# Performance work log

Hardware: AMD Instinct MI355X
Metric: run time of the kernel (lower is better)

Reference implementation:

```python
import jax, jax.numpy as jnp
import numpy as np

KQ_D = 64  # head dim from init_kwargs

def setup_inputs() -> dict:
    key = jax.random.key(0)
    k1, k2, k3, k4 = jax.random.split(key, 4)
    B, H, S, D = 2, 12, 2048, KQ_D
    q = jax.random.normal(k1, (B, H, S, D), dtype=jnp.float32)
    k = jax.random.normal(k2, (B, H, S, D), dtype=jnp.float32)
    v = jax.random.normal(k3, (B, H, S, D), dtype=jnp.float32)
    mask = jax.random.randint(k4, (B, 1, S, S), 0, 2, dtype=jnp.int32)
    return {"q": q, "k": k, "v": v, "mask": mask}

def reference(q, k, v, mask):
    # attn = (q @ k^T) / sqrt(kq_d)
    scale = 1.0 / (KQ_D ** 0.5)
    attn = jnp.einsum('bhqd,bhkd->bhqk', q, k) * scale
    # masked_fill(mask == 0, -1e9)
    attn = jnp.where(mask == 0, jnp.float32(-1e9), attn)
    # softmax over keys; dropout is identity in eval/reference mode
    attn = jax.nn.softmax(attn, axis=-1)
    out = jnp.einsum('bhqk,bhkd->bhqd', attn, v)
    return out
```

## Files before the change

kernel.cpp:

```cpp
#include <hip/hip_runtime.h>
#include <hip/hip_bf16.h>

#define S_LEN 2048
#define D_DIM 64
#define NH    12
#define NB    2
#define BH_N  (NB*NH)
#define TILES 32
#define TILE_BYTES 16384
#define KV_WS_BYTES ((size_t)BH_N * TILES * TILE_BYTES)
#define MASK_WORDS  ((size_t)NB * S_LEN * TILES)
#define WS_NEEDED   (KV_WS_BYTES + MASK_WORDS * 8)

typedef __attribute__((ext_vector_type(8))) short short8;
typedef __attribute__((ext_vector_type(4))) float f32x4;
typedef __attribute__((ext_vector_type(16))) float f32x16;

static __device__ inline unsigned bfbits(float f) {
    __hip_bfloat16 h = __float2bfloat16(f);
    return (unsigned)*reinterpret_cast<const unsigned short*>(&h);
}

static __device__ inline void gload_lds16(const void* g, unsigned ldsoff) {
    __builtin_amdgcn_global_load_lds(
        (__attribute__((address_space(1))) void*)(unsigned long long)(uintptr_t)g,
        (__attribute__((address_space(3))) void*)(unsigned long long)ldsoff,
        16, 0, 0);
}

__global__ __launch_bounds__(256) void prep(const float* __restrict__ k,
                                            const float* __restrict__ v,
                                            const int* __restrict__ mask,
                                            char* __restrict__ wsKV,
                                            unsigned long long* __restrict__ wm) {
    __shared__ __align__(16) float sv[64 * 68];
    const int tid = threadIdx.x;
    const int bid = blockIdx.x;
    if (bid < 768) {
        const int t = bid & 31, bh = bid >> 5;
        const int kv0 = t * 64;
        const float* kb = k + (size_t)bh * (S_LEN * D_DIM);
        const float* vb = v + (size_t)bh * (S_LEN * D_DIM);
        char* img = wsKV + ((size_t)bh * TILES + t) * TILE_BYTES;

#pragma unroll
        for (int g = 0; g < 4; ++g) {
            int i = g * 256 + tid;
            int row = i >> 4, cb = (i & 15) << 3;
            int cp = cb ^ ((row & 7) << 4);
            float4 f = *(const float4*)(kb + (size_t)(kv0 + row) * D_DIM + (cp >> 1));
            uint2 u;
            u.x = bfbits(f.x) | (bfbits(f.y) << 16);
            u.y = bfbits(f.z) | (bfbits(f.w) << 16);
            *(uint2*)(img + (size_t)i * 8) = u;
            float4 fv = *(const float4*)(vb + (size_t)(kv0 + row) * D_DIM + ((i & 15) << 2));
            *(float4*)&sv[row * 68 + ((i & 15) << 2)] = fv;
        }
        __syncthreads();
#pragma unroll
        for (int g = 0; g < 4; ++g) {
            int i = g * 256 + tid;
            int drow = i >> 4, cb = (i & 15) << 3;
            int cp = cb ^ ((drow & 7) << 4);
            int key0 = cp >> 1;
            uint2 u;
            u.x = bfbits(sv[(key0 + 0) * 68 + drow]) | (bfbits(sv[(key0 + 1) * 68 + drow]) << 16);
            u.y = bfbits(sv[(key0 + 2) * 68 + drow]) | (bfbits(sv[(key0 + 3) * 68 + drow]) << 16);
            *(uint2*)(img + 8192 + (size_t)i * 8) = u;
        }
    } else {
        const int lane = tid & 63;
        const int wgid = (bid - 768) * 4 + (tid >> 6);
#pragma unroll 1
        for (int g = 0; g < 16; ++g) {
            const int t0 = wgid * 64 + g * 4;
            const size_t base = (size_t)t0 * 64 + lane;
            int m0 = mask[base];
            int m1 = mask[base + 64];
            int m2 = mask[base + 128];
            int m3 = mask[base + 192];
            unsigned long long b0 = __ballot(m0 != 0);
            unsigned long long b1 = __ballot(m1 != 0);
            unsigned long long b2 = __ballot(m2 != 0);
            unsigned long long b3 = __ballot(m3 != 0);
            if (lane == 0) {
                wm[t0 + 0] = b0; wm[t0 + 1] = b1;
                wm[t0 + 2] = b2; wm[t0 + 3] = b3;
            }
        }
    }
}

__global__ __launch_bounds__(256, 3) void attn_main(
    const float* __restrict__ q, const char* __restrict__ wsKV,
    const unsigned long long* __restrict__ wm, float* __restrict__ out)
{
    __shared__ __align__(16) char smem[2 * TILE_BYTES + 8192];

    const int tid  = threadIdx.x;
    const int wave = tid >> 6;
    const int lane = tid & 63;
    const int l32  = lane & 31;
    const int lh   = lane >> 5;
    const int qh   = wave & 1;
    const int kh   = wave >> 1;

    const int f  = blockIdx.x;
    const int n  = (f & 7) * 96 + (f >> 3);
    const int bx = n & 31;
    const int bh = n >> 5;
    const int b  = bh / NH;
    const int qw = bx * 64 + qh * 32;
    const int qq = qw + l32;

    const float* qb = q + (size_t)bh * (S_LEN * D_DIM);
    float*       ob = out + (size_t)bh * (S_LEN * D_DIM);
    const char*  tileBase = wsKV + (size_t)bh * TILES * TILE_BYTES;
    const size_t widx = ((size_t)b * S_LEN + qq) * TILES;

    const float PRE = 0.125f * 1.44269504088896f;

    short8 bq[4];
#pragma unroll
    for (int c = 0; c < 4; ++c) {
        const float* src = qb + (size_t)qq * D_DIM + c * 16 + lh * 8;
        float4 f0 = *(const float4*)(src);
        float4 f1 = *(const float4*)(src + 4);
        short8 a;
        a[0] = (short)bfbits(f0.x * PRE); a[1] = (short)bfbits(f0.y * PRE);
        a[2] = (short)bfbits(f0.z * PRE); a[3] = (short)bfbits(f0.w * PRE);
        a[4] = (short)bfbits(f1.x * PRE); a[5] = (short)bfbits(f1.y * PRE);
        a[6] = (short)bfbits(f1.z * PRE); a[7] = (short)bfbits(f1.w * PRE);
        bq[c] = a;
    }

    f32x16 o0, o1;
#pragma unroll
    for (int i = 0; i < 16; ++i) { o0[i] = 0.f; o1[i] = 0.f; }
    float lsum = 0.f;

    const unsigned smem_base = (unsigned)(uintptr_t)(&smem[0]);
    char* pw = smem + 2 * TILE_BYTES + wave * 2048;
    const unsigned swzP = (unsigned)((l32 & 3) << 4);
    const int krow = kh * 32 + l32;
    const unsigned kswz = (unsigned)((l32 & 7) << 4);

    unsigned long long mw = wm[widx];
    unsigned long long mwn;
#pragma unroll
    for (int j = 0; j < 4; ++j) {
        unsigned off = (unsigned)(wave * 4096 + j * 1024 + lane * 16);
        gload_lds16(tileBase + off, smem_base + off);
    }
    __syncthreads();

    int buf = 0;
    for (int t = 0; t < 32; ++t) {
        if (t < 31) {
            const char* timg = tileBase + (size_t)(t + 1) * TILE_BYTES;
            unsigned dstb = smem_base + (unsigned)((buf ^ 1) * TILE_BYTES);
#pragma unroll
            for (int j = 0; j < 4; ++j) {
                unsigned off = (unsigned)(wave * 4096 + j * 1024 + lane * 16);
                gload_lds16(timg + off, dstb + off);
            }
            mwn = wm[widx + t + 1];
        }

        const char* sK  = smem + buf * TILE_BYTES;
        const char* sVt = sK + 8192;

        f32x16 sc;
#pragma unroll
        for (int i = 0; i < 16; ++i) sc[i] = 0.f;
#pragma unroll
        for (int c = 0; c < 4; ++c) {
            unsigned byte = (unsigned)(krow * 128) + (((unsigned)(c * 32 + lh * 16)) ^ kswz);
            short8 ak = *(const short8*)(sK + byte);
            sc = __builtin_amdgcn_mfma_f32_32x32x16_bf16(ak, bq[c], sc, 0, 0, 0);
        }

        short8 bv00, bv01, bv10, bv11;
        {
            unsigned d0 = (unsigned)(l32 * 128);
            unsigned d1 = (unsigned)((32 + l32) * 128);
            unsigned c0 = ((unsigned)(kh * 64 + 0 * 32 + lh * 16)) ^ kswz;
            unsigned c1 = ((unsigned)(kh * 64 + 1 * 32 + lh * 16)) ^ kswz;
            bv00 = *(const short8*)(sVt + d0 + c0);
            bv01 = *(const short8*)(sVt + d1 + c0);
            bv10 = *(const short8*)(sVt + d0 + c1);
            bv11 = *(const short8*)(sVt + d1 + c1);
        }

        unsigned mh = (unsigned)(mw >> (kh * 32 + lh * 4));
        float rs = 0.f;
#pragma unroll
        for (int g = 0; g < 4; ++g) {
            unsigned nib = (mh >> (8 * g)) & 0xFu;
            float p0 = (nib & 1u) ? exp2f(sc[4 * g + 0]) : 0.f;
            float p1 = (nib & 2u) ? exp2f(sc[4 * g + 1]) : 0.f;
            float p2 = (nib & 4u) ? exp2f(sc[4 * g + 2]) : 0.f;
            float p3 = (nib & 8u) ? exp2f(sc[4 * g + 3]) : 0.f;
            rs += (p0 + p1) + (p2 + p3);
            uint2 u;
            u.x = bfbits(p0) | (bfbits(p1) << 16);
            u.y = bfbits(p2) | (bfbits(p3) << 16);
            unsigned byte = (unsigned)(l32 * 64) + (((unsigned)(16 * g + 8 * lh)) ^ swzP);
            *(uint2*)(pw + byte) = u;
        }
        lsum += rs;

#pragma unroll
        for (int kc = 0; kc < 2; ++kc) {
            unsigned pbyte = (unsigned)(l32 * 64) + (((unsigned)(kc * 32 + lh * 16)) ^ swzP);
            short8 pa = *(const short8*)(pw + pbyte);
            if (kc == 0) {
                o0 = __builtin_amdgcn_mfma_f32_32x32x16_bf16(pa, bv00, o0, 0, 0, 0);
                o1 = __builtin_amdgcn_mfma_f32_32x32x16_bf16(pa, bv01, o1, 0, 0, 0);
            } else {
                o0 = __builtin_amdgcn_mfma_f32_32x32x16_bf16(pa, bv10, o0, 0, 0, 0);
                o1 = __builtin_amdgcn_mfma_f32_32x32x16_bf16(pa, bv11, o1, 0, 0, 0);
            }
        }

        __syncthreads();
        buf ^= 1;
        mw = mwn;
    }

    float* mO = (float*)smem;
    float* sl = (float*)(smem + 16384);

    lsum += __shfl_xor(lsum, 32);
    if (lh == 0) sl[kh * 64 + qh * 32 + l32] = lsum;
    if (kh == 1) {
#pragma unroll
        for (int g = 0; g < 4; ++g)
#pragma unroll
            for (int r = 0; r < 4; ++r) {
                int reg = 4 * g + r;
                int qrow = r + 8 * g + 4 * lh;
                mO[qh * 2048 + qrow * 64 + l32]      = o0[reg];
                mO[qh * 2048 + qrow * 64 + 32 + l32] = o1[reg];
            }
    }
    __syncthreads();
    if (kh == 0) {
#pragma unroll
        for (int g = 0; g < 4; ++g)
#pragma unroll
            for (int r = 0; r < 4; ++r) {
                int reg = 4 * g + r;
                int qrow = r + 8 * g + 4 * lh;
                float l = sl[qh * 32 + qrow] + sl[64 + qh * 32 + qrow];
                float inv = 1.0f / l;
                float v0 = (o0[reg] + mO[qh * 2048 + qrow * 64 + l32]) * inv;
                float v1 = (o1[reg] + mO[qh * 2048 + qrow * 64 + 32 + l32]) * inv;
                ob[(size_t)(qw + qrow) * D_DIM + l32]      = v0;
                ob[(size_t)(qw + qrow) * D_DIM + 32 + l32] = v1;
            }
    }
}

__global__ __launch_bounds__(256, 3) void attn_fallback(
    const float* __restrict__ q, const float* __restrict__ k,
    const float* __restrict__ v, const int* __restrict__ mask,
    float* __restrict__ out)
{
    __shared__ __align__(16) unsigned short sK[4096];
    __shared__ __align__(16) unsigned short sVt[4096];
    __shared__ __align__(16) unsigned short sP[4096];

    const int tid  = threadIdx.x;
    const int wave = tid >> 6;
    const int lane = tid & 63;
    const int l16  = lane & 15;
    const int lhi  = lane >> 4;

    const int bh = blockIdx.y;
    const int b  = bh / NH;
    const int q0 = blockIdx.x * 64;
    const int qw = q0 + wave * 16;
    const int qq = qw + l16;

    const float* qbase = q + (size_t)bh * S_LEN * D_DIM;
    const float* kbase = k + (size_t)bh * S_LEN * D_DIM;
    const float* vbase = v + (size_t)bh * S_LEN * D_DIM;
    const int*   mp = mask + (size_t)b * S_LEN * S_LEN + (size_t)qq * S_LEN;

    const float PRE = 0.125f * 1.44269504088896f;

    short8 bq[2];
#pragma unroll
    for (int ks = 0; ks < 2; ++ks) {
        const float* src = qbase + (size_t)qq * D_DIM + ks * 32 + lhi * 8;
        float4 f0 = *(const float4*)(src);
        float4 f1 = *(const float4*)(src + 4);
        short8 a;
        a[0] = (short)bfbits(f0.x * PRE); a[1] = (short)bfbits(f0.y * PRE);
        a[2] = (short)bfbits(f0.z * PRE); a[3] = (short)bfbits(f0.w * PRE);
        a[4] = (short)bfbits(f1.x * PRE); a[5] = (short)bfbits(f1.y * PRE);
        a[6] = (short)bfbits(f1.z * PRE); a[7] = (short)bfbits(f1.w * PRE);
        bq[ks] = a;
    }

    f32x4 o[4];
#pragma unroll
    for (int dt = 0; dt < 4; ++dt) o[dt] = (f32x4){0.f, 0.f, 0.f, 0.f};
    float mrun = -1e30f, lrun = 0.f;
    unsigned short* pw = sP + wave * 1024;

    int srow[4], sd[4];
#pragma unroll
    for (int s = 0; s < 4; ++s) { int i = tid + 256 * s; srow[s] = i >> 4; sd[s] = (i & 15) * 4; }

    float4 kreg[4], vreg[4];
#pragma unroll
    for (int s = 0; s < 4; ++s) {
        kreg[s] = *(const float4*)(kbase + (size_t)srow[s] * D_DIM + sd[s]);
        vreg[s] = *(const float4*)(vbase + (size_t)srow[s] * D_DIM + sd[s]);
    }

    for (int kv0 = 0; kv0 < S_LEN; kv0 += 64) {
        __syncthreads();
#pragma unroll
        for (int s = 0; s < 4; ++s) {
            unsigned p0 = bfbits(kreg[s].x) | (bfbits(kreg[s].y) << 16);
            unsigned p1 = bfbits(kreg[s].z) | (bfbits(kreg[s].w) << 16);
            int byte = srow[s] * 128 + ((sd[s] * 2) ^ ((srow[s] & 7) << 4));
            *(uint2*)((char*)sK + byte) = make_uint2(p0, p1);
        }
#pragma unroll
        for (int s = 0; s < 4; ++s) {
            float ff[4] = {vreg[s].x, vreg[s].y, vreg[s].z, vreg[s].w};
#pragma unroll
            for (int jj = 0; jj < 4; ++jj) {
                int dd = sd[s] + jj;
                int byte = dd * 128 + ((srow[s] * 2) ^ ((dd & 7) << 4));
                *(unsigned short*)((char*)sVt + byte) = (unsigned short)bfbits(ff[jj]);
            }
        }
        __syncthreads();

        if (kv0 + 64 < S_LEN) {
#pragma unroll
            for (int s = 0; s < 4; ++s) {
                kreg[s] = *(const float4*)(kbase + (size_t)(kv0 + 64 + srow[s]) * D_DIM + sd[s]);
                vreg[s] = *(const float4*)(vbase + (size_t)(kv0 + 64 + srow[s]) * D_DIM + sd[s]);
            }
        }

        int4 m0 = *(const int4*)(mp + kv0 + lhi * 4);
        int4 m1 = *(const int4*)(mp + kv0 + 16 + lhi * 4);
        int4 m2 = *(const int4*)(mp + kv0 + 32 + lhi * 4);
        int4 m3 = *(const int4*)(mp + kv0 + 48 + lhi * 4);

        f32x4 sc[4];
#pragma unroll
        for (int tt = 0; tt < 4; ++tt) sc[tt] = (f32x4){0.f, 0.f, 0.f, 0.f};
#pragma unroll
        for (int ks = 0; ks < 2; ++ks) {
#pragma unroll
            for (int tt = 0; tt < 4; ++tt) {
                int row = tt * 16 + l16;
                int byte = row * 128 + ((ks * 64 + lhi * 16) ^ ((row & 7) << 4));
                short8 ak = *(const short8*)((const char*)sK + byte);
                sc[tt] = __builtin_amdgcn_mfma_f32_16x16x32_bf16(ak, bq[ks], sc[tt], 0, 0, 0);
            }
        }

        const int4 mm[4] = {m0, m1, m2, m3};
        float pm = -1e30f;
#pragma unroll
        for (int tt = 0; tt < 4; ++tt)
#pragma unroll
            for (int r = 0; r < 4; ++r) {
                float s = ((const int*)&mm[tt])[r] ? sc[tt][r] : -1e9f;
                sc[tt][r] = s;
                pm = fmaxf(pm, s);
            }
        pm = fmaxf(pm, __shfl_xor(pm, 16));
        pm = fmaxf(pm, __shfl_xor(pm, 32));

        float mnew = fmaxf(mrun, pm);
        float fsc = exp2f(mrun - mnew);
        mrun = mnew;
        float rs = 0.f;
#pragma unroll
        for (int tt = 0; tt < 4; ++tt)
#pragma unroll
            for (int r = 0; r < 4; ++r) {
                float p = exp2f(sc[tt][r] - mnew);
                sc[tt][r] = p;
                rs += p;
            }
        rs += __shfl_xor(rs, 16);
        rs += __shfl_xor(rs, 32);
        lrun = lrun * fsc + rs;

        float fr[4];
#pragma unroll
        for (int r = 0; r < 4; ++r) fr[r] = __shfl(fsc, lhi * 4 + r);
#pragma unroll
        for (int dt = 0; dt < 4; ++dt)
#pragma unroll
            for (int r = 0; r < 4; ++r) o[dt][r] *= fr[r];

#pragma unroll
        for (int tt = 0; tt < 4; ++tt) {
            unsigned p0 = bfbits(sc[tt][0]) | (bfbits(sc[tt][1]) << 16);
            unsigned p1 = bfbits(sc[tt][2]) | (bfbits(sc[tt][3]) << 16);
            int byte = l16 * 128 + (((tt * 16 + lhi * 4) * 2) ^ ((l16 & 7) << 4));
            *(uint2*)((char*)pw + byte) = make_uint2(p0, p1);
        }

#pragma unroll
        for (int ks = 0; ks < 2; ++ks) {
            int pbyte = l16 * 128 + ((ks * 64 + lhi * 16) ^ ((l16 & 7) << 4));
            short8 pa = *(const short8*)((const char*)pw + pbyte);
#pragma unroll
            for (int dt = 0; dt < 4; ++dt) {
                int drow = dt * 16 + l16;
                int vbyte = drow * 128 + ((ks * 64 + lhi * 16) ^ ((drow & 7) << 4));
                short8 bv = *(const short8*)((const char*)sVt + vbyte);
                o[dt] = __builtin_amdgcn_mfma_f32_16x16x32_bf16(pa, bv, o[dt], 0, 0, 0);
            }
        }
    }

    float invl = 1.0f / lrun;
    float ir[4];
#pragma unroll
    for (int r = 0; r < 4; ++r) ir[r] = __shfl(invl, lhi * 4 + r);
#pragma unroll
    for (int dt = 0; dt < 4; ++dt)
#pragma unroll
        for (int r = 0; r < 4; ++r) {
            int qrow = qw + lhi * 4 + r;
            int dcol = dt * 16 + l16;
            out[(size_t)bh * S_LEN * D_DIM + (size_t)qrow * D_DIM + dcol] = o[dt][r] * ir[r];
        }
}

extern "C" void kernel_launch(void* const* d_in, const int* in_sizes, int n_in,
                              void* d_out, int out_size, void* d_ws, size_t ws_size,
                              hipStream_t stream) {
    const float* q   = (const float*)d_in[0];
    const float* k   = (const float*)d_in[1];
    const float* v   = (const float*)d_in[2];
    const int* mask  = (const int*)d_in[3];
    float* out = (float*)d_out;

    if (ws_size >= WS_NEEDED) {
        char* ws = (char*)d_ws;
        char* wsKV = ws;
        unsigned long long* wm = (unsigned long long*)(ws + KV_WS_BYTES);
        prep<<<dim3(1280), dim3(256), 0, stream>>>(k, v, mask, wsKV, wm);
        attn_main<<<dim3(768), dim3(256), 0, stream>>>(q, wsKV, wm, out);
    } else {
        attn_fallback<<<dim3(S_LEN / 64, BH_N), dim3(256), 0, stream>>>(q, k, v, mask, out);
    }
}
```

Measured before the change: 81.60 us.

## Repack softmax probabilities in registers via permlane32 swap instead of LDS

Replaces the per-wave LDS round trip for the bf16 probability tile (store, then reload as MFMA A operand) with in-register packing and v_permlane32_swap to move data between lane halves. This drops 8 KB of shared memory per block and the LDS write/read latency. It also changes the K/V tile swizzle to a 16-row XOR pattern (SWZ) in both prep and the consumer, to reduce bank conflicts. The lane-exchange layout must exactly match the MFMA operand layout, which adds a correctness risk.

```diff
diff --git a/kernel.cpp b/kernel.cpp
--- a/kernel.cpp
+++ b/kernel.cpp
@@ -15,6 +15,7 @@
 typedef __attribute__((ext_vector_type(8))) short short8;
 typedef __attribute__((ext_vector_type(4))) float f32x4;
 typedef __attribute__((ext_vector_type(16))) float f32x16;
+typedef __attribute__((ext_vector_type(2))) int iv2;
 
 static __device__ inline unsigned bfbits(float f) {
     __hip_bfloat16 h = __float2bfloat16(f);
@@ -27,6 +28,8 @@
         (__attribute__((address_space(3))) void*)(unsigned long long)ldsoff,
         16, 0, 0);
 }
+
+#define SWZ(r) ((((r) & 7) << 4) ^ (((r) & 8) << 2))
 
 __global__ __launch_bounds__(256) void prep(const float* __restrict__ k,
                                             const float* __restrict__ v,
@@ -47,7 +50,7 @@
         for (int g = 0; g < 4; ++g) {
             int i = g * 256 + tid;
             int row = i >> 4, cb = (i & 15) << 3;
-            int cp = cb ^ ((row & 7) << 4);
+            int cp = cb ^ SWZ(row);
             float4 f = *(const float4*)(kb + (size_t)(kv0 + row) * D_DIM + (cp >> 1));
             uint2 u;
             u.x = bfbits(f.x) | (bfbits(f.y) << 16);
@@ -61,7 +64,7 @@
         for (int g = 0; g < 4; ++g) {
             int i = g * 256 + tid;
             int drow = i >> 4, cb = (i & 15) << 3;
-            int cp = cb ^ ((drow & 7) << 4);
+            int cp = cb ^ SWZ(drow);
             int key0 = cp >> 1;
             uint2 u;
             u.x = bfbits(sv[(key0 + 0) * 68 + drow]) | (bfbits(sv[(key0 + 1) * 68 + drow]) << 16);
@@ -95,7 +98,7 @@
     const float* __restrict__ q, const char* __restrict__ wsKV,
     const unsigned long long* __restrict__ wm, float* __restrict__ out)
 {
-    __shared__ __align__(16) char smem[2 * TILE_BYTES + 8192];
+    __shared__ __align__(16) char smem[2 * TILE_BYTES];
 
     const int tid  = threadIdx.x;
     const int wave = tid >> 6;
@@ -140,10 +143,8 @@
     float lsum = 0.f;
 
     const unsigned smem_base = (unsigned)(uintptr_t)(&smem[0]);
-    char* pw = smem + 2 * TILE_BYTES + wave * 2048;
-    const unsigned swzP = (unsigned)((l32 & 3) << 4);
     const int krow = kh * 32 + l32;
-    const unsigned kswz = (unsigned)((l32 & 7) << 4);
+    const unsigned kswz = (unsigned)SWZ(l32);
 
     unsigned long long mw = wm[widx];
     unsigned long long mwn;
@@ -193,35 +194,47 @@
         }
 
         unsigned mh = (unsigned)(mw >> (kh * 32 + lh * 4));
-        float rs = 0.f;
+        float p[16];
 #pragma unroll
         for (int g = 0; g < 4; ++g) {
             unsigned nib = (mh >> (8 * g)) & 0xFu;
-            float p0 = (nib & 1u) ? exp2f(sc[4 * g + 0]) : 0.f;
-            float p1 = (nib & 2u) ? exp2f(sc[4 * g + 1]) : 0.f;
-            float p2 = (nib & 4u) ? exp2f(sc[4 * g + 2]) : 0.f;
-            float p3 = (nib & 8u) ? exp2f(sc[4 * g + 3]) : 0.f;
-            rs += (p0 + p1) + (p2 + p3);
-            uint2 u;
-            u.x = bfbits(p0) | (bfbits(p1) << 16);
-            u.y = bfbits(p2) | (bfbits(p3) << 16);
-            unsigned byte = (unsigned)(l32 * 64) + (((unsigned)(16 * g + 8 * lh)) ^ swzP);
-            *(uint2*)(pw + byte) = u;
-        }
-        lsum += rs;
-
-#pragma unroll
-        for (int kc = 0; kc < 2; ++kc) {
-            unsigned pbyte = (unsigned)(l32 * 64) + (((unsigned)(kc * 32 + lh * 16)) ^ swzP);
-            short8 pa = *(const short8*)(pw + pbyte);
-            if (kc == 0) {
-                o0 = __builtin_amdgcn_mfma_f32_32x32x16_bf16(pa, bv00, o0, 0, 0, 0);
-                o1 = __builtin_amdgcn_mfma_f32_32x32x16_bf16(pa, bv01, o1, 0, 0, 0);
-            } else {
-                o0 = __builtin_amdgcn_mfma_f32_32x32x16_bf16(pa, bv10, o0, 0, 0, 0);
-                o1 = __builtin_amdgcn_mfma_f32_32x32x16_bf16(pa, bv11, o1, 0, 0, 0);
-            }
-        }
+            p[4*g+0] = (nib & 1u) ? exp2f(sc[4*g+0]) : 0.f;
+            p[4*g+1] = (nib & 2u) ? exp2f(sc[4*g+1]) : 0.f;
+            p[4*g+2] = (nib & 4u) ? exp2f(sc[4*g+2]) : 0.f;
+            p[4*g+3] = (nib & 8u) ? exp2f(sc[4*g+3]) : 0.f;
+        }
+        {
+            float s0 = (p[0] + p[1]) + (p[2] + p[3]);
+            float s1 = (p[4] + p[5]) + (p[6] + p[7]);
+            float s2 = (p[8] + p[9]) + (p[10] + p[11]);
+            float s3 = (p[12] + p[13]) + (p[14] + p[15]);
+            lsum += (s0 + s1) + (s2 + s3);
+        }
+
+        unsigned w01 = bfbits(p[0])  | (bfbits(p[1])  << 16);
+        unsigned w23 = bfbits(p[2])  | (bfbits(p[3])  << 16);
+        unsigned w45 = bfbits(p[4])  | (bfbits(p[5])  << 16);
+        unsigned w67 = bfbits(p[6])  | (bfbits(p[7])  << 16);
+        unsigned w89 = bfbits(p[8])  | (bfbits(p[9])  << 16);
+        unsigned wAB = bfbits(p[10]) | (bfbits(p[11]) << 16);
+        unsigned wCD = bfbits(p[12]) | (bfbits(p[13]) << 16);
+        unsigned wEF = bfbits(p[14]) | (bfbits(p[15]) << 16);
+        iv2 r0 = __builtin_amdgcn_permlane32_swap((int)w01, (int)w45, false, false);
+        iv2 r1 = __builtin_amdgcn_permlane32_swap((int)w23, (int)w67, false, false);
+        iv2 r2 = __builtin_amdgcn_permlane32_swap((int)w89, (int)wCD, false, false);
+        iv2 r3 = __builtin_amdgcn_permlane32_swap((int)wAB, (int)wEF, false, false);
+        uint4 ua0, ua1;
+        ua0.x = (unsigned)r0[0]; ua0.y = (unsigned)r1[0];
+        ua0.z = (unsigned)r0[1]; ua0.w = (unsigned)r1[1];
+        ua1.x = (unsigned)r2[0]; ua1.y = (unsigned)r3[0];
+        ua1.z = (unsigned)r2[1]; ua1.w = (unsigned)r3[1];
+        short8 pa0 = *reinterpret_cast<short8*>(&ua0);
+        short8 pa1 = *reinterpret_cast<short8*>(&ua1);
+
+        o0 = __builtin_amdgcn_mfma_f32_32x32x16_bf16(pa0, bv00, o0, 0, 0, 0);
+        o1 = __builtin_amdgcn_mfma_f32_32x32x16_bf16(pa0, bv01, o1, 0, 0, 0);
+        o0 = __builtin_amdgcn_mfma_f32_32x32x16_bf16(pa1, bv10, o0, 0, 0, 0);
+        o1 = __builtin_amdgcn_mfma_f32_32x32x16_bf16(pa1, bv11, o1, 0, 0, 0);
 
         __syncthreads();
         buf ^= 1;
```

Measured after the change: 77.90 us. 1.05x faster.
